# Kernel optimization log

Hardware: AMD Instinct MI355X
Metric: run time of the kernel (lower is better)

## Reference

```python
import jax, jax.numpy as jnp
import numpy as np

B, N, D = 8, 2048, 512


def setup_inputs() -> dict:
    key = jax.random.key(0)
    ks = jax.random.split(key, 5)
    bound = 1.0 / np.sqrt(D)
    return {
        "query": jax.random.normal(ks[0], (B, N, D), dtype=jnp.float32),
        "context": jax.random.normal(ks[1], (B, N, D), dtype=jnp.float32),
        "Wq": jax.random.uniform(ks[2], (D, D), minval=-bound, maxval=bound, dtype=jnp.float32),
        "bq": jnp.zeros((D,), dtype=jnp.float32),
        "Wv": jax.random.uniform(ks[3], (D, D), minval=-bound, maxval=bound, dtype=jnp.float32),
        "bv": jnp.zeros((D,), dtype=jnp.float32),
        "Wo": jax.random.uniform(ks[4], (D, D), minval=-bound, maxval=bound, dtype=jnp.float32),
        "bo": jnp.zeros((D,), dtype=jnp.float32),
    }


def reference(query, context, Wq, bq, Wv, bv, Wo, bo):
    d = query.shape[-1]
    scale = 1.0 / jnp.sqrt(jnp.asarray(d, dtype=query.dtype))
    # Linear projections (eqx.nn.Linear: y = W @ x + b -> x @ W.T + b)
    q = jnp.einsum("bnd,ed->bne", query, Wq) + bq      # (B, N, D)
    v = jnp.einsum("bnd,ed->bne", context, Wv) + bv    # (B, N, D)
    # NOTE: original module computes scores against RAW context (key layer unused)
    scores = jnp.einsum("bqd,bkd->bqk", q, context) * scale  # (B, N, N)
    attn = jax.nn.softmax(scores, axis=-1)
    h = jnp.einsum("bqk,bkd->bqd", attn, v)            # (B, N, D)
    return jnp.einsum("bnd,ed->bne", h, Wo) + bo
```

## Files before the change

### kernel.cpp

```cpp
#include <hip/hip_runtime.h>
#include <math.h>

#define NB  8
#define SEQ 2048
#define DIM 512

typedef short v8s __attribute__((ext_vector_type(8)));
typedef float v4f __attribute__((ext_vector_type(4)));

__device__ __forceinline__ unsigned short f2bf(float f) {
    unsigned int u = __float_as_uint(f);
    u += 0x7fffu + ((u >> 16) & 1u);
    return (unsigned short)(u >> 16);
}
__device__ __forceinline__ float bf2f(unsigned short h) {
    return __uint_as_float((unsigned int)h << 16);
}
__device__ __forceinline__ void async16(const unsigned short* g, unsigned short* l) {
    __builtin_amdgcn_global_load_lds(
        (const __attribute__((address_space(1))) unsigned int*)g,
        (__attribute__((address_space(3))) unsigned int*)l, 16, 0, 0);
}

__global__ __launch_bounds__(256)
void conv_bf16(const float* __restrict__ x, unsigned short* __restrict__ y)
{
    int i = blockIdx.x * 256 + threadIdx.x;
    float4 v = ((const float4*)x)[i];
    ushort4 o; o.x = f2bf(v.x); o.y = f2bf(v.y); o.z = f2bf(v.z); o.w = f2bf(v.w);
    ((ushort4*)y)[i] = o;
}

template<int MODE>
__global__ __launch_bounds__(256, 2)
void proj_sgl(const unsigned short* __restrict__ Xbf, const float* __restrict__ W,
              const float* __restrict__ bias, unsigned short* __restrict__ Y)
{
    __shared__ __align__(16) unsigned short As[128 * 64];
    __shared__ __align__(16) unsigned short Bs[128 * 64];

    const int t = threadIdx.x, wave = t >> 6, lane = t & 63;
    const int l15 = lane & 15, quad = lane >> 4;
    const int m0 = blockIdx.x * 128, e0 = blockIdx.y * 128;

    v4f hacc[2][8];
#pragma unroll
    for (int mt = 0; mt < 2; mt++)
#pragma unroll
        for (int nt = 0; nt < 8; nt++) hacc[mt][nt] = (v4f){0.f, 0.f, 0.f, 0.f};

    const int lr8 = lane >> 3, lc8 = lane & 7;

#define STAGE_A(bk)                                                            \
    _Pragma("unroll") for (int i = 0; i < 4; i++) {                            \
        int row = wave * 32 + i * 8 + lr8;                                     \
        int lc = lc8 ^ (row & 7);                                              \
        async16(Xbf + (size_t)(m0 + row) * DIM + (bk) * 64 + lc * 8,           \
                &As[(wave * 32 + i * 8) * 64]);                                \
    }
#define STAGE_B(bk)                                                            \
    _Pragma("unroll") for (int j = 0; j < 8; j++) {                            \
        int u = t * 8 + j;                                                     \
        int row = u >> 4, c4 = u & 15;                                         \
        float4 wv = *(const float4*)(W + (size_t)(e0 + row) * DIM + (bk) * 64 + c4 * 4); \
        ushort4 o = make_ushort4(f2bf(wv.x), f2bf(wv.y), f2bf(wv.z), f2bf(wv.w)); \
        int sc = (c4 >> 1) ^ (row & 7);                                        \
        *(ushort4*)&Bs[row * 64 + sc * 8 + (c4 & 1) * 4] = o;                  \
    }

    STAGE_A(0) STAGE_B(0)
    for (int bk = 0; bk < 8; bk++) {
        __syncthreads();
#pragma unroll
        for (int kc = 0; kc < 2; kc++) {
            v8s a[2];
#pragma unroll
            for (int mt = 0; mt < 2; mt++) {
                int row = wave * 32 + mt * 16 + l15;
                a[mt] = *(const v8s*)&As[row * 64 + (((kc * 4 + quad) ^ (row & 7)) * 8)];
            }
#pragma unroll
            for (int nt = 0; nt < 8; nt++) {
                int er = nt * 16 + l15;
                v8s bfr = *(const v8s*)&Bs[er * 64 + (((kc * 4 + quad) ^ (er & 7)) * 8)];
#pragma unroll
                for (int mt = 0; mt < 2; mt++)
                    hacc[mt][nt] = __builtin_amdgcn_mfma_f32_16x16x32_bf16(a[mt], bfr, hacc[mt][nt], 0, 0, 0);
            }
        }
        __syncthreads();
        if (bk + 1 < 8) { STAGE_A(bk + 1) STAGE_B(bk + 1) }
    }
#undef STAGE_A
#undef STAGE_B

#pragma unroll
    for (int mt = 0; mt < 2; mt++)
#pragma unroll
        for (int nt = 0; nt < 8; nt++) {
            int col = e0 + nt * 16 + l15;
            float bb = bias[col];
            if (MODE == 0) {
#pragma unroll
                for (int r = 0; r < 4; r++) {
                    int row = m0 + wave * 32 + mt * 16 + quad * 4 + r;
                    Y[(size_t)row * DIM + col] = f2bf(hacc[mt][nt][r] + bb);
                }
            } else {
                int rowb = m0 + wave * 32 + mt * 16 + quad * 4;
                int bidx = rowb >> 11, n = rowb & 2047;
                ushort4 o = make_ushort4(f2bf(hacc[mt][nt][0] + bb), f2bf(hacc[mt][nt][1] + bb),
                                         f2bf(hacc[mt][nt][2] + bb), f2bf(hacc[mt][nt][3] + bb));
                *(ushort4*)&Y[(size_t)bidx * DIM * SEQ + (size_t)col * SEQ + n] = o;
            }
        }
}

__global__ __launch_bounds__(256, 2)
void proj_split(const unsigned short* __restrict__ Ahi, const unsigned short* __restrict__ Alo,
                const float* __restrict__ W, const float* __restrict__ bias,
                float* __restrict__ Y)
{
    __shared__ __align__(16) unsigned short Ah[128 * 64];
    __shared__ __align__(16) unsigned short Al[128 * 64];
    __shared__ __align__(16) unsigned short Bh[128 * 64];
    __shared__ __align__(16) unsigned short Bl[128 * 64];

    const int t = threadIdx.x, wave = t >> 6, lane = t & 63;
    const int l15 = lane & 15, quad = lane >> 4;
    const int m0 = blockIdx.x * 128, e0 = blockIdx.y * 128;

    v4f hacc[2][8];
#pragma unroll
    for (int mt = 0; mt < 2; mt++)
#pragma unroll
        for (int nt = 0; nt < 8; nt++) hacc[mt][nt] = (v4f){0.f, 0.f, 0.f, 0.f};

    const int lr8 = lane >> 3, lc8 = lane & 7;

#define STAGE_A2(bk)                                                           \
    _Pragma("unroll") for (int i = 0; i < 4; i++) {                            \
        int row = wave * 32 + i * 8 + lr8;                                     \
        int lc = lc8 ^ (row & 7);                                              \
        size_t ga = (size_t)(m0 + row) * DIM + (bk) * 64 + lc * 8;             \
        async16(Ahi + ga, &Ah[(wave * 32 + i * 8) * 64]);                      \
        async16(Alo + ga, &Al[(wave * 32 + i * 8) * 64]);                      \
    }
#define STAGE_B2(bk)                                                           \
    _Pragma("unroll") for (int j = 0; j < 8; j++) {                            \
        int u = t * 8 + j;                                                     \
        int row = u >> 4, c4 = u & 15;                                         \
        float4 wv = *(const float4*)(W + (size_t)(e0 + row) * DIM + (bk) * 64 + c4 * 4); \
        ushort4 oh = make_ushort4(f2bf(wv.x), f2bf(wv.y), f2bf(wv.z), f2bf(wv.w)); \
        ushort4 ol = make_ushort4(f2bf(wv.x - bf2f(oh.x)), f2bf(wv.y - bf2f(oh.y)), \
                                  f2bf(wv.z - bf2f(oh.z)), f2bf(wv.w - bf2f(oh.w))); \
        int sc = (c4 >> 1) ^ (row & 7);                                        \
        int sa = row * 64 + sc * 8 + (c4 & 1) * 4;                             \
        *(ushort4*)&Bh[sa] = oh;                                               \
        *(ushort4*)&Bl[sa] = ol;                                               \
    }

    STAGE_A2(0) STAGE_B2(0)
    for (int bk = 0; bk < 8; bk++) {
        __syncthreads();
#pragma unroll
        for (int kc = 0; kc < 2; kc++) {
            v8s ah[2], al[2];
#pragma unroll
            for (int mt = 0; mt < 2; mt++) {
                int row = wave * 32 + mt * 16 + l15;
                int sa = row * 64 + (((kc * 4 + quad) ^ (row & 7)) * 8);
                ah[mt] = *(const v8s*)&Ah[sa];
                al[mt] = *(const v8s*)&Al[sa];
            }
#pragma unroll
            for (int nt = 0; nt < 8; nt++) {
                int er = nt * 16 + l15;
                int sb = er * 64 + (((kc * 4 + quad) ^ (er & 7)) * 8);
                v8s bh = *(const v8s*)&Bh[sb];
                v8s bl = *(const v8s*)&Bl[sb];
#pragma unroll
                for (int mt = 0; mt < 2; mt++) {
                    hacc[mt][nt] = __builtin_amdgcn_mfma_f32_16x16x32_bf16(ah[mt], bh, hacc[mt][nt], 0, 0, 0);
                    hacc[mt][nt] = __builtin_amdgcn_mfma_f32_16x16x32_bf16(al[mt], bh, hacc[mt][nt], 0, 0, 0);
                    hacc[mt][nt] = __builtin_amdgcn_mfma_f32_16x16x32_bf16(ah[mt], bl, hacc[mt][nt], 0, 0, 0);
                }
            }
        }
        __syncthreads();
        if (bk + 1 < 8) { STAGE_A2(bk + 1) STAGE_B2(bk + 1) }
    }
#undef STAGE_A2
#undef STAGE_B2

#pragma unroll
    for (int mt = 0; mt < 2; mt++)
#pragma unroll
        for (int nt = 0; nt < 8; nt++) {
            int col = e0 + nt * 16 + l15;
            float bb = bias[col];
#pragma unroll
            for (int r = 0; r < 4; r++) {
                int row = m0 + wave * 32 + mt * 16 + quad * 4 + r;
                Y[(size_t)row * DIM + col] = hacc[mt][nt][r] + bb;
            }
        }
}

__global__ __launch_bounds__(512, 2)
void flash_mfma2(const unsigned short* __restrict__ qbf,
                 const unsigned short* __restrict__ ctxbf,
                 const unsigned short* __restrict__ vT,
                 unsigned short* __restrict__ hhi,
                 unsigned short* __restrict__ hlo)
{
    __shared__ __align__(16) unsigned short Ks[64 * 512];
    __shared__ __align__(16) unsigned short Ps[64 * 72];
    __shared__ __align__(16) float Sf[64 * 68];
    __shared__ float alphaS[64];

    const int t = threadIdx.x;
    const int wave = t >> 6, lane = t & 63;
    const int l15 = lane & 15, quad = lane >> 4;
    const int strip = wave & 3, half = wave >> 2;
    const int lr = lane >> 3, l8 = lane & 7;
    const int b = blockIdx.y, m0 = blockIdx.x * 64;

    const unsigned short* ctxb = ctxbf + (size_t)b * SEQ * DIM;
    const unsigned short* vTb  = vT    + (size_t)b * DIM * SEQ;
    const float scale = 0.044194173824159216f;

    v8s qf[16];
    {
        const unsigned short* qrow = qbf + ((size_t)b * SEQ + m0 + strip * 16 + l15) * DIM;
#pragma unroll
        for (int kc = 0; kc < 16; kc++)
            qf[kc] = *(const v8s*)(qrow + kc * 32 + quad * 8);
    }
    v4f hacc[4][4];
#pragma unroll
    for (int m = 0; m < 4; m++)
#pragma unroll
        for (int dt = 0; dt < 4; dt++) hacc[m][dt] = (v4f){0.f, 0.f, 0.f, 0.f};

    float M = -INFINITY, L = 0.f;

#pragma unroll
    for (int i = 0; i < 8; i++) {
        int row = wave * 8 + i;
        async16(ctxb + (size_t)row * DIM + (size_t)(lane ^ (row & 7)) * 8, &Ks[row * 512]);
    }

    for (int kt = 0; kt < SEQ / 64; kt++) {
        __syncthreads();
        v8s vf[4][2];
#pragma unroll
        for (int dt = 0; dt < 4; dt++)
#pragma unroll
            for (int kc = 0; kc < 2; kc++)
                vf[dt][kc] = *(const v8s*)(vTb + (size_t)(wave * 64 + dt * 16 + l15) * SEQ
                                           + kt * 64 + kc * 32 + quad * 8);
        v4f sacc[2];
        sacc[0] = (v4f){0.f, 0.f, 0.f, 0.f};
        sacc[1] = (v4f){0.f, 0.f, 0.f, 0.f};
#pragma unroll
        for (int kc = 0; kc < 16; kc++) {
#pragma unroll
            for (int ct = 0; ct < 2; ct++) {
                int key = half * 32 + ct * 16 + l15;
                v8s kf = *(const v8s*)&Ks[key * 512 + (((kc * 4 + quad) ^ (key & 7)) * 8)];
                sacc[ct] = __builtin_amdgcn_mfma_f32_16x16x32_bf16(qf[kc], kf, sacc[ct], 0, 0, 0);
            }
        }
#pragma unroll
        for (int ct = 0; ct < 2; ct++)
#pragma unroll
            for (int r = 0; r < 4; r++)
                Sf[(strip * 16 + quad * 4 + r) * 68 + half * 32 + ct * 16 + l15] = sacc[ct][r] * scale;
        __syncthreads();
        {
            int row = wave * 8 + lr;
            float sv[8];
            *(float4*)&sv[0] = *(const float4*)&Sf[row * 68 + l8 * 8];
            *(float4*)&sv[4] = *(const float4*)&Sf[row * 68 + l8 * 8 + 4];
            float mx = sv[0];
#pragma unroll
            for (int j = 1; j < 8; j++) mx = fmaxf(mx, sv[j]);
#pragma unroll
            for (int off = 1; off < 8; off <<= 1) mx = fmaxf(mx, __shfl_xor(mx, off, 64));
            float Mn = fmaxf(M, mx);
            float al = __expf(M - Mn);
            float sm = 0.f;
            v8s pv;
#pragma unroll
            for (int j = 0; j < 8; j++) {
                float p = __expf(sv[j] - Mn);
                sm += p;
                pv[j] = (short)f2bf(p);
            }
#pragma unroll
            for (int off = 1; off < 8; off <<= 1) sm += __shfl_xor(sm, off, 64);
            L = L * al + sm;
            M = Mn;
            *(v8s*)&Ps[row * 72 + l8 * 8] = pv;
            if (l8 == 0) alphaS[row] = al;
        }
        __syncthreads();
        if (kt + 1 < SEQ / 64) {
#pragma unroll
            for (int i = 0; i < 8; i++) {
                int row = wave * 8 + i;
                async16(ctxb + (size_t)((kt + 1) * 64 + row) * DIM + (size_t)(lane ^ (row & 7)) * 8,
                        &Ks[row * 512]);
            }
        }
#pragma unroll
        for (int m = 0; m < 4; m++) {
            v4f a4;
#pragma unroll
            for (int r = 0; r < 4; r++) a4[r] = alphaS[m * 16 + quad * 4 + r];
#pragma unroll
            for (int dt = 0; dt < 4; dt++) hacc[m][dt] *= a4;
        }
#pragma unroll
        for (int kc = 0; kc < 2; kc++) {
            v8s pa[4];
#pragma unroll
            for (int m = 0; m < 4; m++)
                pa[m] = *(const v8s*)&Ps[(m * 16 + l15) * 72 + kc * 32 + quad * 8];
#pragma unroll
            for (int dt = 0; dt < 4; dt++)
#pragma unroll
                for (int m = 0; m < 4; m++)
                    hacc[m][dt] = __builtin_amdgcn_mfma_f32_16x16x32_bf16(pa[m], vf[dt][kc], hacc[m][dt], 0, 0, 0);
        }
    }

    __syncthreads();
    if (l8 == 0) alphaS[wave * 8 + lr] = 1.0f / L;
    __syncthreads();
#pragma unroll
    for (int m = 0; m < 4; m++) {
#pragma unroll
        for (int r = 0; r < 4; r++) {
            float invL = alphaS[m * 16 + quad * 4 + r];
            int grow = m0 + m * 16 + quad * 4 + r;
#pragma unroll
            for (int dt = 0; dt < 4; dt++) {
                float o = hacc[m][dt][r] * invL;
                unsigned short hi = f2bf(o);
                float lof = o - bf2f(hi);
                size_t idx = ((size_t)b * SEQ + grow) * DIM + wave * 64 + dt * 16 + l15;
                hhi[idx] = hi;
                hlo[idx] = f2bf(lof);
            }
        }
    }
}

extern "C" void kernel_launch(void* const* d_in, const int* in_sizes, int n_in,
                              void* d_out, int out_size, void* d_ws, size_t ws_size,
                              hipStream_t stream)
{
    const float* query   = (const float*)d_in[0];
    const float* context = (const float*)d_in[1];
    const float* Wq      = (const float*)d_in[2];
    const float* bq      = (const float*)d_in[3];
    const float* Wv      = (const float*)d_in[4];
    const float* bv      = (const float*)d_in[5];
    const float* Wo      = (const float*)d_in[6];
    const float* bo      = (const float*)d_in[7];

    const size_t NE = (size_t)NB * SEQ * DIM;
    unsigned short* qbf = (unsigned short*)d_ws;
    unsigned short* cbf = qbf + NE;
    unsigned short* hhi = cbf + NE;
    unsigned short* hlo = hhi + NE;
    unsigned short* vTb = (unsigned short*)d_out;
    unsigned short* qx  = ((unsigned short*)d_out) + NE;

    dim3 gridP(128, 4);

    conv_bf16   <<<NE / 1024, 256, 0, stream>>>(query, qx);
    conv_bf16   <<<NE / 1024, 256, 0, stream>>>(context, cbf);
    proj_sgl<0> <<<gridP, 256, 0, stream>>>(qx,  Wq, bq, qbf);
    proj_sgl<1> <<<gridP, 256, 0, stream>>>(cbf, Wv, bv, vTb);
    flash_mfma2 <<<dim3(SEQ / 64, NB), 512, 0, stream>>>(qbf, cbf, vTb, hhi, hlo);
    proj_split  <<<gridP, 256, 0, stream>>>(hhi, hlo, Wo, bo, (float*)d_out);
}
```

Baseline: 345.8 us.

## Shrink flash tile to 32 queries with split-D score partials

The attention kernel now handles 32 query rows and 32 keys per block instead of 64x64. The QK^T dot product is split across two wave groups along the feature dimension, and the partial score tiles are summed in shared memory. The grid is swapped so batch varies fastest, LDS use shrinks, and launch bounds ask for 4 blocks per CU, all aiming for more resident blocks and better latency hiding. In exchange there are twice as many key iterations with three barriers each, and V^T and K tiles are reloaded for every 32-row query block, doubling that global traffic.

```diff
diff --git a/kernel.cpp b/kernel.cpp
--- a/kernel.cpp
+++ b/kernel.cpp
@@ -207,140 +207,128 @@
         }
 }
 
-__global__ __launch_bounds__(512, 2)
-void flash_mfma2(const unsigned short* __restrict__ qbf,
+__global__ __launch_bounds__(512, 4)
+void flash_mfma3(const unsigned short* __restrict__ qbf,
                  const unsigned short* __restrict__ ctxbf,
                  const unsigned short* __restrict__ vT,
                  unsigned short* __restrict__ hhi,
                  unsigned short* __restrict__ hlo)
 {
-    __shared__ __align__(16) unsigned short Ks[64 * 512];
-    __shared__ __align__(16) unsigned short Ps[64 * 72];
-    __shared__ __align__(16) float Sf[64 * 68];
-    __shared__ float alphaS[64];
+    __shared__ __align__(16) unsigned short Ks[32 * 512];
+    __shared__ __align__(16) unsigned short Ps[32 * 64];
+    __shared__ __align__(16) float Sf[2 * 32 * 36];
+    __shared__ float alphaS[32];
 
     const int t = threadIdx.x;
     const int wave = t >> 6, lane = t & 63;
     const int l15 = lane & 15, quad = lane >> 4;
-    const int strip = wave & 3, half = wave >> 2;
-    const int lr = lane >> 3, l8 = lane & 7;
-    const int b = blockIdx.y, m0 = blockIdx.x * 64;
+    const int qs = wave & 1, kh = (wave >> 1) & 1, dh = wave >> 2;
+    const int srow = t >> 4;
+    const int b = blockIdx.x, m0 = blockIdx.y * 32;
 
     const unsigned short* ctxb = ctxbf + (size_t)b * SEQ * DIM;
     const unsigned short* vTb  = vT    + (size_t)b * DIM * SEQ;
     const float scale = 0.044194173824159216f;
 
-    v8s qf[16];
+    v8s qf[8];
     {
-        const unsigned short* qrow = qbf + ((size_t)b * SEQ + m0 + strip * 16 + l15) * DIM;
-#pragma unroll
-        for (int kc = 0; kc < 16; kc++)
+        const unsigned short* qrow = qbf + ((size_t)b * SEQ + m0 + qs * 16 + l15) * DIM + dh * 256;
+#pragma unroll
+        for (int kc = 0; kc < 8; kc++)
             qf[kc] = *(const v8s*)(qrow + kc * 32 + quad * 8);
     }
-    v4f hacc[4][4];
-#pragma unroll
-    for (int m = 0; m < 4; m++)
+
+    v4f hacc[2][4];
+#pragma unroll
+    for (int m = 0; m < 2; m++)
 #pragma unroll
         for (int dt = 0; dt < 4; dt++) hacc[m][dt] = (v4f){0.f, 0.f, 0.f, 0.f};
 
     float M = -INFINITY, L = 0.f;
 
 #pragma unroll
-    for (int i = 0; i < 8; i++) {
-        int row = wave * 8 + i;
+    for (int i = 0; i < 4; i++) {
+        int row = wave * 4 + i;
         async16(ctxb + (size_t)row * DIM + (size_t)(lane ^ (row & 7)) * 8, &Ks[row * 512]);
     }
 
-    for (int kt = 0; kt < SEQ / 64; kt++) {
-        __syncthreads();
-        v8s vf[4][2];
+    for (int kt = 0; kt < SEQ / 32; kt++) {
+        __syncthreads();
+        v8s vf[4];
 #pragma unroll
         for (int dt = 0; dt < 4; dt++)
-#pragma unroll
-            for (int kc = 0; kc < 2; kc++)
-                vf[dt][kc] = *(const v8s*)(vTb + (size_t)(wave * 64 + dt * 16 + l15) * SEQ
-                                           + kt * 64 + kc * 32 + quad * 8);
-        v4f sacc[2];
-        sacc[0] = (v4f){0.f, 0.f, 0.f, 0.f};
-        sacc[1] = (v4f){0.f, 0.f, 0.f, 0.f};
-#pragma unroll
-        for (int kc = 0; kc < 16; kc++) {
-#pragma unroll
-            for (int ct = 0; ct < 2; ct++) {
-                int key = half * 32 + ct * 16 + l15;
-                v8s kf = *(const v8s*)&Ks[key * 512 + (((kc * 4 + quad) ^ (key & 7)) * 8)];
-                sacc[ct] = __builtin_amdgcn_mfma_f32_16x16x32_bf16(qf[kc], kf, sacc[ct], 0, 0, 0);
-            }
-        }
-#pragma unroll
-        for (int ct = 0; ct < 2; ct++)
-#pragma unroll
-            for (int r = 0; r < 4; r++)
-                Sf[(strip * 16 + quad * 4 + r) * 68 + half * 32 + ct * 16 + l15] = sacc[ct][r] * scale;
-        __syncthreads();
+            vf[dt] = *(const v8s*)(vTb + (size_t)(wave * 64 + dt * 16 + l15) * SEQ
+                                   + kt * 32 + quad * 8);
+        v4f sacc = (v4f){0.f, 0.f, 0.f, 0.f};
         {
-            int row = wave * 8 + lr;
-            float sv[8];
-            *(float4*)&sv[0] = *(const float4*)&Sf[row * 68 + l8 * 8];
-            *(float4*)&sv[4] = *(const float4*)&Sf[row * 68 + l8 * 8 + 4];
-            float mx = sv[0];
-#pragma unroll
-            for (int j = 1; j < 8; j++) mx = fmaxf(mx, sv[j]);
-#pragma unroll
-            for (int off = 1; off < 8; off <<= 1) mx = fmaxf(mx, __shfl_xor(mx, off, 64));
+            const int key = kh * 16 + l15;
+#pragma unroll
+            for (int kc = 0; kc < 8; kc++) {
+                v8s kf = *(const v8s*)&Ks[key * 512 + (((dh * 32 + kc * 4 + quad) ^ (key & 7)) * 8)];
+                sacc = __builtin_amdgcn_mfma_f32_16x16x32_bf16(qf[kc], kf, sacc, 0, 0, 0);
+            }
+        }
+        {
+            float* sf = &Sf[(dh * 32 + qs * 16 + quad * 4) * 36 + kh * 16 + l15];
+#pragma unroll
+            for (int r = 0; r < 4; r++) sf[r * 36] = sacc[r] * scale;
+        }
+        __syncthreads();
+        {
+            float2 a0 = *(const float2*)&Sf[srow * 36 + 2 * l15];
+            float2 a1 = *(const float2*)&Sf[(32 + srow) * 36 + 2 * l15];
+            float s0 = a0.x + a1.x, s1 = a0.y + a1.y;
+            float mx = fmaxf(s0, s1);
+#pragma unroll
+            for (int off = 1; off < 16; off <<= 1) mx = fmaxf(mx, __shfl_xor(mx, off, 64));
             float Mn = fmaxf(M, mx);
             float al = __expf(M - Mn);
-            float sm = 0.f;
-            v8s pv;
-#pragma unroll
-            for (int j = 0; j < 8; j++) {
-                float p = __expf(sv[j] - Mn);
-                sm += p;
-                pv[j] = (short)f2bf(p);
-            }
-#pragma unroll
-            for (int off = 1; off < 8; off <<= 1) sm += __shfl_xor(sm, off, 64);
+            float p0 = __expf(s0 - Mn), p1 = __expf(s1 - Mn);
+            float sm = p0 + p1;
+#pragma unroll
+            for (int off = 1; off < 16; off <<= 1) sm += __shfl_xor(sm, off, 64);
             L = L * al + sm;
             M = Mn;
-            *(v8s*)&Ps[row * 72 + l8 * 8] = pv;
-            if (l8 == 0) alphaS[row] = al;
-        }
-        __syncthreads();
-        if (kt + 1 < SEQ / 64) {
-#pragma unroll
-            for (int i = 0; i < 8; i++) {
-                int row = wave * 8 + i;
-                async16(ctxb + (size_t)((kt + 1) * 64 + row) * DIM + (size_t)(lane ^ (row & 7)) * 8,
+            int c = (l15 >> 2) ^ (srow & 7);
+            unsigned int pw = (unsigned int)f2bf(p0) | ((unsigned int)f2bf(p1) << 16);
+            *(unsigned int*)&Ps[srow * 64 + c * 8 + 2 * (l15 & 3)] = pw;
+            if (l15 == 0) alphaS[srow] = al;
+        }
+        __syncthreads();
+        if (kt + 1 < SEQ / 32) {
+#pragma unroll
+            for (int i = 0; i < 4; i++) {
+                int row = wave * 4 + i;
+                async16(ctxb + (size_t)((kt + 1) * 32 + row) * DIM + (size_t)(lane ^ (row & 7)) * 8,
                         &Ks[row * 512]);
             }
         }
 #pragma unroll
-        for (int m = 0; m < 4; m++) {
+        for (int m = 0; m < 2; m++) {
             v4f a4;
 #pragma unroll
             for (int r = 0; r < 4; r++) a4[r] = alphaS[m * 16 + quad * 4 + r];
 #pragma unroll
             for (int dt = 0; dt < 4; dt++) hacc[m][dt] *= a4;
         }
-#pragma unroll
-        for (int kc = 0; kc < 2; kc++) {
-            v8s pa[4];
-#pragma unroll
-            for (int m = 0; m < 4; m++)
-                pa[m] = *(const v8s*)&Ps[(m * 16 + l15) * 72 + kc * 32 + quad * 8];
-#pragma unroll
-            for (int dt = 0; dt < 4; dt++)
-#pragma unroll
-                for (int m = 0; m < 4; m++)
-                    hacc[m][dt] = __builtin_amdgcn_mfma_f32_16x16x32_bf16(pa[m], vf[dt][kc], hacc[m][dt], 0, 0, 0);
-        }
+        v8s pa[2];
+#pragma unroll
+        for (int m = 0; m < 2; m++) {
+            int row = m * 16 + l15;
+            pa[m] = *(const v8s*)&Ps[row * 64 + ((quad ^ (row & 7)) * 8)];
+        }
+#pragma unroll
+        for (int dt = 0; dt < 4; dt++)
+#pragma unroll
+            for (int m = 0; m < 2; m++)
+                hacc[m][dt] = __builtin_amdgcn_mfma_f32_16x16x32_bf16(pa[m], vf[dt], hacc[m][dt], 0, 0, 0);
     }
 
     __syncthreads();
-    if (l8 == 0) alphaS[wave * 8 + lr] = 1.0f / L;
+    if (l15 == 0) alphaS[srow] = 1.0f / L;
     __syncthreads();
 #pragma unroll
-    for (int m = 0; m < 4; m++) {
+    for (int m = 0; m < 2; m++) {
 #pragma unroll
         for (int r = 0; r < 4; r++) {
             float invL = alphaS[m * 16 + quad * 4 + r];
@@ -385,6 +373,6 @@
     conv_bf16   <<<NE / 1024, 256, 0, stream>>>(context, cbf);
     proj_sgl<0> <<<gridP, 256, 0, stream>>>(qx,  Wq, bq, qbf);
     proj_sgl<1> <<<gridP, 256, 0, stream>>>(cbf, Wv, bv, vTb);
-    flash_mfma2 <<<dim3(SEQ / 64, NB), 512, 0, stream>>>(qbf, cbf, vTb, hhi, hlo);
+    flash_mfma3 <<<dim3(NB, SEQ / 32), 512, 0, stream>>>(qbf, cbf, vTb, hhi, hlo);
     proj_split  <<<gridP, 256, 0, stream>>>(hhi, hlo, Wo, bo, (float*)d_out);
 }
```

Result: slower. 430.8 us (+24.6%).

## Compute softmax in registers, shrink LDS, raise occupancy in flash kernel

Applied to the files above, without the earlier changes.

Softmax now runs directly on the MFMA accumulator registers, using cross-lane shuffles plus a small per-half max/sum exchange in LDS. This replaces staging the full score tile in LDS and reducing it there. The Sf buffer and P padding are dropped (P uses an XOR swizzle instead), and launch bounds are raised to 4 blocks per CU. Other changes: the V loads move later to shorten register live ranges, s_setprio is placed around the MFMA phases, and the grid is reordered so blocks of the same batch are interleaved differently. Risks are register pressure from the tighter launch bounds causing spills, and the extra barrier-separated exchange.

```diff
diff --git a/kernel.cpp b/kernel.cpp
--- a/kernel.cpp
+++ b/kernel.cpp
@@ -207,24 +207,25 @@
         }
 }
 
-__global__ __launch_bounds__(512, 2)
-void flash_mfma2(const unsigned short* __restrict__ qbf,
+__global__ __launch_bounds__(512, 4)
+void flash_mfma4(const unsigned short* __restrict__ qbf,
                  const unsigned short* __restrict__ ctxbf,
                  const unsigned short* __restrict__ vT,
                  unsigned short* __restrict__ hhi,
                  unsigned short* __restrict__ hlo)
 {
     __shared__ __align__(16) unsigned short Ks[64 * 512];
-    __shared__ __align__(16) unsigned short Ps[64 * 72];
-    __shared__ __align__(16) float Sf[64 * 68];
+    __shared__ __align__(16) unsigned short Ps[64 * 64];
+    __shared__ float Mp[2][64];
+    __shared__ float Sp[2][64];
     __shared__ float alphaS[64];
 
     const int t = threadIdx.x;
     const int wave = t >> 6, lane = t & 63;
     const int l15 = lane & 15, quad = lane >> 4;
     const int strip = wave & 3, half = wave >> 2;
-    const int lr = lane >> 3, l8 = lane & 7;
-    const int b = blockIdx.y, m0 = blockIdx.x * 64;
+    const int qrow0 = strip * 16 + quad * 4;
+    const int b = blockIdx.x, m0 = blockIdx.y * 64;
 
     const unsigned short* ctxb = ctxbf + (size_t)b * SEQ * DIM;
     const unsigned short* vTb  = vT    + (size_t)b * DIM * SEQ;
@@ -243,7 +244,9 @@
 #pragma unroll
         for (int dt = 0; dt < 4; dt++) hacc[m][dt] = (v4f){0.f, 0.f, 0.f, 0.f};
 
-    float M = -INFINITY, L = 0.f;
+    float M[4], L[4];
+#pragma unroll
+    for (int r = 0; r < 4; r++) { M[r] = -INFINITY; L[r] = 0.f; }
 
 #pragma unroll
     for (int i = 0; i < 8; i++) {
@@ -253,16 +256,10 @@
 
     for (int kt = 0; kt < SEQ / 64; kt++) {
         __syncthreads();
-        v8s vf[4][2];
-#pragma unroll
-        for (int dt = 0; dt < 4; dt++)
-#pragma unroll
-            for (int kc = 0; kc < 2; kc++)
-                vf[dt][kc] = *(const v8s*)(vTb + (size_t)(wave * 64 + dt * 16 + l15) * SEQ
-                                           + kt * 64 + kc * 32 + quad * 8);
         v4f sacc[2];
         sacc[0] = (v4f){0.f, 0.f, 0.f, 0.f};
         sacc[1] = (v4f){0.f, 0.f, 0.f, 0.f};
+        __builtin_amdgcn_s_setprio(1);
 #pragma unroll
         for (int kc = 0; kc < 16; kc++) {
 #pragma unroll
@@ -272,40 +269,58 @@
                 sacc[ct] = __builtin_amdgcn_mfma_f32_16x16x32_bf16(qf[kc], kf, sacc[ct], 0, 0, 0);
             }
         }
-#pragma unroll
-        for (int ct = 0; ct < 2; ct++)
+        __builtin_amdgcn_s_setprio(0);
+        float s0[4], s1[4], mx[4];
+#pragma unroll
+        for (int r = 0; r < 4; r++) {
+            s0[r] = sacc[0][r] * scale;
+            s1[r] = sacc[1][r] * scale;
+            mx[r] = fmaxf(s0[r], s1[r]);
+        }
+#pragma unroll
+        for (int off = 1; off < 16; off <<= 1)
 #pragma unroll
             for (int r = 0; r < 4; r++)
-                Sf[(strip * 16 + quad * 4 + r) * 68 + half * 32 + ct * 16 + l15] = sacc[ct][r] * scale;
-        __syncthreads();
-        {
-            int row = wave * 8 + lr;
-            float sv[8];
-            *(float4*)&sv[0] = *(const float4*)&Sf[row * 68 + l8 * 8];
-            *(float4*)&sv[4] = *(const float4*)&Sf[row * 68 + l8 * 8 + 4];
-            float mx = sv[0];
-#pragma unroll
-            for (int j = 1; j < 8; j++) mx = fmaxf(mx, sv[j]);
-#pragma unroll
-            for (int off = 1; off < 8; off <<= 1) mx = fmaxf(mx, __shfl_xor(mx, off, 64));
-            float Mn = fmaxf(M, mx);
-            float al = __expf(M - Mn);
-            float sm = 0.f;
-            v8s pv;
-#pragma unroll
-            for (int j = 0; j < 8; j++) {
-                float p = __expf(sv[j] - Mn);
-                sm += p;
-                pv[j] = (short)f2bf(p);
-            }
-#pragma unroll
-            for (int off = 1; off < 8; off <<= 1) sm += __shfl_xor(sm, off, 64);
-            L = L * al + sm;
-            M = Mn;
-            *(v8s*)&Ps[row * 72 + l8 * 8] = pv;
-            if (l8 == 0) alphaS[row] = al;
-        }
-        __syncthreads();
+                mx[r] = fmaxf(mx[r], __shfl_xor(mx[r], off, 64));
+        if (l15 == 0) {
+#pragma unroll
+            for (int r = 0; r < 4; r++) Mp[half][qrow0 + r] = mx[r];
+        }
+        __syncthreads();
+        float Mn[4], al[4], sm[4];
+#pragma unroll
+        for (int r = 0; r < 4; r++) {
+            float mo = fmaxf(Mp[0][qrow0 + r], Mp[1][qrow0 + r]);
+            Mn[r] = fmaxf(M[r], mo);
+            al[r] = __expf(M[r] - Mn[r]);
+            float p0 = __expf(s0[r] - Mn[r]);
+            float p1 = __expf(s1[r] - Mn[r]);
+            sm[r] = p0 + p1;
+            int row = qrow0 + r;
+            int k0 = half * 32 + l15;
+            int k1 = k0 + 16;
+            Ps[row * 64 + (((k0 >> 3) ^ (row & 7)) << 3) + (k0 & 7)] = f2bf(p0);
+            Ps[row * 64 + (((k1 >> 3) ^ (row & 7)) << 3) + (k1 & 7)] = f2bf(p1);
+        }
+#pragma unroll
+        for (int off = 1; off < 16; off <<= 1)
+#pragma unroll
+            for (int r = 0; r < 4; r++)
+                sm[r] += __shfl_xor(sm[r], off, 64);
+        if (l15 == 0) {
+#pragma unroll
+            for (int r = 0; r < 4; r++) Sp[half][qrow0 + r] = sm[r];
+            if (half == 0) {
+#pragma unroll
+                for (int r = 0; r < 4; r++) alphaS[qrow0 + r] = al[r];
+            }
+        }
+        __syncthreads();
+#pragma unroll
+        for (int r = 0; r < 4; r++) {
+            L[r] = L[r] * al[r] + Sp[0][qrow0 + r] + Sp[1][qrow0 + r];
+            M[r] = Mn[r];
+        }
         if (kt + 1 < SEQ / 64) {
 #pragma unroll
             for (int i = 0; i < 8; i++) {
@@ -314,6 +329,13 @@
                         &Ks[row * 512]);
             }
         }
+        v8s vf[4][2];
+#pragma unroll
+        for (int dt = 0; dt < 4; dt++)
+#pragma unroll
+            for (int kc2 = 0; kc2 < 2; kc2++)
+                vf[dt][kc2] = *(const v8s*)(vTb + (size_t)(wave * 64 + dt * 16 + l15) * SEQ
+                                            + kt * 64 + kc2 * 32 + quad * 8);
 #pragma unroll
         for (int m = 0; m < 4; m++) {
             v4f a4;
@@ -322,22 +344,25 @@
 #pragma unroll
             for (int dt = 0; dt < 4; dt++) hacc[m][dt] *= a4;
         }
-#pragma unroll
-        for (int kc = 0; kc < 2; kc++) {
-            v8s pa[4];
-#pragma unroll
-            for (int m = 0; m < 4; m++)
-                pa[m] = *(const v8s*)&Ps[(m * 16 + l15) * 72 + kc * 32 + quad * 8];
-#pragma unroll
-            for (int dt = 0; dt < 4; dt++)
-#pragma unroll
-                for (int m = 0; m < 4; m++)
-                    hacc[m][dt] = __builtin_amdgcn_mfma_f32_16x16x32_bf16(pa[m], vf[dt][kc], hacc[m][dt], 0, 0, 0);
-        }
+        __builtin_amdgcn_s_setprio(1);
+#pragma unroll
+        for (int kc2 = 0; kc2 < 2; kc2++)
+#pragma unroll
+            for (int m = 0; m < 4; m++) {
+                int row = m * 16 + l15;
+                v8s pa = *(const v8s*)&Ps[row * 64 + (((kc2 * 4 + quad) ^ (row & 7)) << 3)];
+#pragma unroll
+                for (int dt = 0; dt < 4; dt++)
+                    hacc[m][dt] = __builtin_amdgcn_mfma_f32_16x16x32_bf16(pa, vf[dt][kc2], hacc[m][dt], 0, 0, 0);
+            }
+        __builtin_amdgcn_s_setprio(0);
     }
 
     __syncthreads();
-    if (l8 == 0) alphaS[wave * 8 + lr] = 1.0f / L;
+    if (half == 0 && l15 == 0) {
+#pragma unroll
+        for (int r = 0; r < 4; r++) alphaS[qrow0 + r] = 1.0f / L[r];
+    }
     __syncthreads();
 #pragma unroll
     for (int m = 0; m < 4; m++) {
@@ -385,6 +410,6 @@
     conv_bf16   <<<NE / 1024, 256, 0, stream>>>(context, cbf);
     proj_sgl<0> <<<gridP, 256, 0, stream>>>(qx,  Wq, bq, qbf);
     proj_sgl<1> <<<gridP, 256, 0, stream>>>(cbf, Wv, bv, vTb);
-    flash_mfma2 <<<dim3(SEQ / 64, NB), 512, 0, stream>>>(qbf, cbf, vTb, hhi, hlo);
+    flash_mfma4 <<<dim3(NB, SEQ / 64), 512, 0, stream>>>(qbf, cbf, vTb, hhi, hlo);
     proj_split  <<<gridP, 256, 0, stream>>>(hhi, hlo, Wo, bo, (float*)d_out);
 }
```

Measured after the change: 724.0 us. 2.09x slower.
